# Kernel optimization log

Hardware: AMD Instinct MI355X
Metric: run time of the kernel (lower is better)

## Reference

```python
import jax, jax.numpy as jnp
import numpy as np

SIGMA_S = 1.0
SIGMA_R = 0.1
FR = int(np.ceil(3 * SIGMA_S))          # 3
K_SIZE = 2 * FR + 1                     # 7
B, C, H, W = 8, 3, 512, 512


def matlab_style_gauss2d(shape, sigma):
    m, n = [(ss - 1.0) / 2.0 for ss in shape]
    y, x = np.ogrid[-m:m + 1, -n:n + 1]
    h = np.exp(-(x * x + y * y) / (2.0 * sigma * sigma))
    h[h < np.finfo(h.dtype).eps * h.max()] = 0
    s = h.sum()
    if s != 0:
        h /= s
    return h.astype(np.float32)


GAUSS = matlab_style_gauss2d((K_SIZE, K_SIZE), SIGMA_S)  # [7,7]


def setup_inputs() -> dict:
    key = jax.random.key(0)
    x = jax.random.uniform(key, (B, C, H, W), dtype=jnp.float32)
    return {"input": x}


def reference(input) -> jnp.ndarray:
    # ReflectionPad2d(fr)
    padded = jnp.pad(input, ((0, 0), (0, 0), (FR, FR), (FR, FR)), mode="reflect")
    inv_2sr2 = 1.0 / (2.0 * SIGMA_R * SIGMA_R)
    loss_map = jnp.zeros_like(input)
    for k in range(K_SIZE):
        for l in range(K_SIZE):
            shifted = padded[:, :, k:k + H, l:l + W]            # [B,C,H,W]
            d = input - shifted
            # bilateral range weight * gaussian spatial weight (constant, as in
            # the original which stores weight_map as a raw non-grad tensor)
            w = jax.lax.stop_gradient(
                jnp.exp(-(d * d).sum(1, keepdims=True) * inv_2sr2) * GAUSS[k, l]
            )                                                    # [B,1,H,W]
            loss_map = loss_map + jnp.abs(d) * w
    return loss_map.mean()
```

## Files before the change

### kernel.cpp

```cpp
#include <hip/hip_runtime.h>

#define FR 3
#define KS 7
#define TLX 64
#define TLY 16
#define HX (TLX + 2*FR)
#define HY (TLY + FR)
#define LSTR 72
#define IMG_H 512
#define IMG_W 512
#define NB 8
#define NC 3
#define GXB (IMG_W / TLX)
#define GYB (IMG_H / TLY)
#define NMAIN (GXB * GYB * NB)
#define RIM_PER_IMG 6108
#define NRIM_THREADS (RIM_PER_IMG * NB)
#define NRIM_BLK ((NRIM_THREADS + 255) / 256)
#define NBLK_A (NMAIN + NRIM_BLK)
#define NPART NBLK_A

#define KSC 8.493218f
#define K2F 72.134752f

constexpr double g1d[KS] = {0.011108996538242306, 0.1353352832366127,
                            0.6065306597126334,   1.0,
                            0.6065306597126334,   0.1353352832366127,
                            0.011108996538242306};
constexpr double SUMG = 1.0 + 2.0 * (0.011108996538242306 + 0.1353352832366127
                                     + 0.6065306597126334);
constexpr double INVN = 1.0 / (SUMG * SUMG);
constexpr double KD   = 8.493218;
constexpr double WPAIR = 2.0 * INVN / KD;

__device__ __forceinline__ int refl(int i, int n) {
    i = (i < 0) ? -i : i;
    return (i >= n) ? (2*n - 2 - i) : i;
}

__global__ __launch_bounds__(256) void blt_fused(const float* __restrict__ in,
                                                 float* __restrict__ partial) {
    __shared__ float sm[NC][HY][LSTR];
    __shared__ float wsum[4];
    const int tid = threadIdx.x;
    float a = 0.0f;

    if (blockIdx.x >= NRIM_BLK) {
        const int bid = blockIdx.x - NRIM_BLK;
        const int b   = bid >> 8;
        const int rem = bid & 255;
        const int byi = rem >> 3;
        const int bxi = rem & 7;
        const int by  = byi * TLY;
        const int bx  = bxi * TLX;
        const int tx  = tid & 31;
        const int ty  = tid >> 5;
        const float* base = in + (size_t)b * NC * IMG_H * IMG_W;

        for (int idx = tid; idx < HY * HX; idx += 256) {
            int ly = idx / HX;
            int lx = idx - ly * HX;
            int gy = refl(by + ly - FR, IMG_H);
            int gx = refl(bx + lx - FR, IMG_W);
            #pragma unroll
            for (int c = 0; c < NC; ++c)
                sm[c][ly][lx] = base[(c * IMG_H + gy) * IMG_W + gx] * KSC;
        }
        __syncthreads();

        const int r0 = ty * 2;
        float cc[NC][2][2];

        if ((bxi != 0) & (bxi != GXB - 1) & (byi != 0)) {
            #pragma unroll
            for (int rr = 4; rr >= 0; --rr) {
                float w[NC][8];
                #pragma unroll
                for (int c = 0; c < NC; ++c) {
                    const float2* rp = reinterpret_cast<const float2*>(&sm[c][r0 + rr][2 * tx]);
                    float2 p0 = rp[0], p1 = rp[1], p2 = rp[2], p3 = rp[3];
                    w[c][0] = p0.x; w[c][1] = p0.y; w[c][2] = p1.x; w[c][3] = p1.y;
                    w[c][4] = p2.x; w[c][5] = p2.y; w[c][6] = p3.x; w[c][7] = p3.y;
                }
                #pragma unroll
                for (int i = 0; i < 2; ++i) {
                    const int k = rr - i;
                    if (k < 0 || k > FR) continue;
                    if (k == FR) {
                        #pragma unroll
                        for (int c = 0; c < NC; ++c) {
                            cc[c][i][0] = w[c][3];
                            cc[c][i][1] = w[c][4];
                        }
                    }
                    const int lmax = (k == FR) ? FR : KS;
                    #pragma unroll
                    for (int j = 0; j < 2; ++j) {
                        #pragma unroll
                        for (int l = 0; l < KS; ++l) {
                            if (l >= lmax) continue;
                            float d0 = cc[0][i][j] - w[0][l + j];
                            float d1 = cc[1][i][j] - w[1][l + j];
                            float d2 = cc[2][i][j] - w[2][l + j];
                            float s = d0 * d0;
                            s = fmaf(d1, d1, s);
                            s = fmaf(d2, d2, s);
                            float e = __builtin_amdgcn_exp2f(-s);
                            float sa = fabsf(d0) + fabsf(d1);
                            sa += fabsf(d2);
                            a = fmaf(sa, e * (float)(g1d[k] * g1d[l] * WPAIR), a);
                        }
                    }
                }
            }
        } else {
            const int x0 = bx + 2 * tx;
            float glm0[KS], glm1[KS];
            #pragma unroll
            for (int l = 0; l < KS; ++l) {
                glm0[l] = ((unsigned)(x0 + l - FR)     < (unsigned)IMG_W) ? (float)(g1d[l] * WPAIR) : 0.0f;
                glm1[l] = ((unsigned)(x0 + 1 + l - FR) < (unsigned)IMG_W) ? (float)(g1d[l] * WPAIR) : 0.0f;
            }
            #pragma unroll
            for (int rr = 4; rr >= 0; --rr) {
                float w[NC][8];
                #pragma unroll
                for (int c = 0; c < NC; ++c) {
                    const float2* rp = reinterpret_cast<const float2*>(&sm[c][r0 + rr][2 * tx]);
                    float2 p0 = rp[0], p1 = rp[1], p2 = rp[2], p3 = rp[3];
                    w[c][0] = p0.x; w[c][1] = p0.y; w[c][2] = p1.x; w[c][3] = p1.y;
                    w[c][4] = p2.x; w[c][5] = p2.y; w[c][6] = p3.x; w[c][7] = p3.y;
                }
                #pragma unroll
                for (int i = 0; i < 2; ++i) {
                    const int k = rr - i;
                    if (k < 0 || k > FR) continue;
                    if (k == FR) {
                        #pragma unroll
                        for (int c = 0; c < NC; ++c) {
                            cc[c][i][0] = w[c][3];
                            cc[c][i][1] = w[c][4];
                        }
                    }
                    const int lmax = (k == FR) ? FR : KS;
                    const float rw = (by + r0 + rr >= FR) ? (float)g1d[k] : 0.0f;
                    float t0 = 0.0f, t1 = 0.0f;
                    #pragma unroll
                    for (int l = 0; l < KS; ++l) {
                        if (l >= lmax) continue;
                        {
                            float d0 = cc[0][i][0] - w[0][l];
                            float d1 = cc[1][i][0] - w[1][l];
                            float d2 = cc[2][i][0] - w[2][l];
                            float s = d0 * d0;
                            s = fmaf(d1, d1, s);
                            s = fmaf(d2, d2, s);
                            float e = __builtin_amdgcn_exp2f(-s);
                            float sa = fabsf(d0) + fabsf(d1);
                            sa += fabsf(d2);
                            t0 = fmaf(sa, e * glm0[l], t0);
                        }
                        {
                            float d0 = cc[0][i][1] - w[0][l + 1];
                            float d1 = cc[1][i][1] - w[1][l + 1];
                            float d2 = cc[2][i][1] - w[2][l + 1];
                            float s = d0 * d0;
                            s = fmaf(d1, d1, s);
                            s = fmaf(d2, d2, s);
                            float e = __builtin_amdgcn_exp2f(-s);
                            float sa = fabsf(d0) + fabsf(d1);
                            sa += fabsf(d2);
                            t1 = fmaf(sa, e * glm1[l], t1);
                        }
                    }
                    a = fmaf(t0, rw, a);
                    a = fmaf(t1, rw, a);
                }
            }
        }
    } else {
        const int idx = blockIdx.x * 256 + tid;
        if (idx < NRIM_THREADS) {
            const int b = idx / RIM_PER_IMG;
            int r = idx - b * RIM_PER_IMG;
            int y, x;
            if (r < 3 * IMG_W) { y = r >> 9; x = r & (IMG_W - 1); }
            else if (r < 6 * IMG_W) { r -= 3 * IMG_W; y = (IMG_H - 3) + (r >> 9); x = r & (IMG_W - 1); }
            else if (r < 6 * IMG_W + 3 * (IMG_H - 6)) { r -= 6 * IMG_W; y = 3 + r / 3; x = r - 3 * (r / 3); }
            else { r -= 6 * IMG_W + 3 * (IMG_H - 6); y = 3 + r / 3; x = (IMG_W - 3) + (r - 3 * (r / 3)); }

            const float* base = in + (size_t)b * NC * IMG_H * IMG_W;
            const float cc0 = base[(0 * IMG_H + y) * IMG_W + x];
            const float cc1 = base[(1 * IMG_H + y) * IMG_W + x];
            const float cc2 = base[(2 * IMG_H + y) * IMG_W + x];

            #pragma unroll
            for (int k = 0; k < KS; ++k) {
                #pragma unroll
                for (int l = 0; l < KS; ++l) {
                    if (k == FR && l == FR) continue;
                    int qy = y + k - FR, qx = x + l - FR;
                    bool oob = ((unsigned)qy >= (unsigned)IMG_H) | ((unsigned)qx >= (unsigned)IMG_W);
                    if (oob) {
                        int ry = refl(qy, IMG_H), rx = refl(qx, IMG_W);
                        float v0 = base[(0 * IMG_H + ry) * IMG_W + rx];
                        float v1 = base[(1 * IMG_H + ry) * IMG_W + rx];
                        float v2 = base[(2 * IMG_H + ry) * IMG_W + rx];
                        float d0 = cc0 - v0, d1 = cc1 - v1, d2 = cc2 - v2;
                        float s = d0 * d0;
                        s = fmaf(d1, d1, s);
                        s = fmaf(d2, d2, s);
                        float e = __builtin_amdgcn_exp2f(-(K2F * s));
                        float sa = fabsf(d0) + fabsf(d1) + fabsf(d2);
                        a = fmaf(sa, e * (float)(g1d[k] * g1d[l] * INVN), a);
                    }
                }
            }
        }
        __syncthreads();
    }

    #pragma unroll
    for (int off = 32; off > 0; off >>= 1)
        a += __shfl_down(a, off, 64);
    if ((tid & 63) == 0) wsum[tid >> 6] = a;
    __syncthreads();
    if (tid == 0)
        partial[blockIdx.x] = wsum[0] + wsum[1] + wsum[2] + wsum[3];
}

__global__ __launch_bounds__(256) void finalize_kernel(const float* __restrict__ partial,
                                                       float* __restrict__ out) {
    __shared__ float wsum[4];
    const int tid = threadIdx.x;
    float a = 0.0f;
    for (int i = tid; i < NPART; i += 256) a += partial[i];
    #pragma unroll
    for (int off = 32; off > 0; off >>= 1)
        a += __shfl_down(a, off, 64);
    if ((tid & 63) == 0) wsum[tid >> 6] = a;
    __syncthreads();
    if (tid == 0)
        out[0] = (wsum[0] + wsum[1] + wsum[2] + wsum[3]) / (float)(NB * NC * IMG_H * IMG_W);
}

extern "C" void kernel_launch(void* const* d_in, const int* in_sizes, int n_in,
                              void* d_out, int out_size, void* d_ws, size_t ws_size,
                              hipStream_t stream) {
    const float* in = (const float*)d_in[0];
    float* out = (float*)d_out;
    float* ws  = (float*)d_ws;

    blt_fused<<<NBLK_A, 256, 0, stream>>>(in, ws);
    finalize_kernel<<<1, 256, 0, stream>>>(ws, out);
}
```

Baseline: 90.95 us.

## Group taps by symmetric weight class and fuse final reduction via atomics

In the interior path, per-tap products are accumulated into ten symmetry-class accumulators and multiplied by the class weight once at the end, removing a multiply per tap. The separate finalize kernel is replaced by a global float atomicAdd plus a completion counter, with the last block writing the mean. A hipMemsetAsync is added to clear the accumulator and counter each call. Float atomics make the summation order nondeterministic, and the memset adds its own launch.

```diff
diff --git a/kernel.cpp b/kernel.cpp
--- a/kernel.cpp
+++ b/kernel.cpp
@@ -18,7 +18,6 @@
 #define NRIM_THREADS (RIM_PER_IMG * NB)
 #define NRIM_BLK ((NRIM_THREADS + 255) / 256)
 #define NBLK_A (NMAIN + NRIM_BLK)
-#define NPART NBLK_A
 
 #define KSC 8.493218f
 #define K2F 72.134752f
@@ -33,13 +32,30 @@
 constexpr double KD   = 8.493218;
 constexpr double WPAIR = 2.0 * INVN / KD;
 
+__host__ __device__ constexpr int clsid(int k, int l) {
+    int a = FR - k;
+    int b = (l < FR) ? (FR - l) : (l - FR);
+    int x = a > b ? a : b, y = a > b ? b : a;
+    return x * (x + 1) / 2 + y;
+}
+__host__ __device__ constexpr double gabs(int a) {
+    return (a == 0) ? 1.0 : (a == 1) ? 0.6065306597126334
+         : (a == 2) ? 0.1353352832366127 : 0.011108996538242306;
+}
+__host__ __device__ constexpr double clsw(int id) {
+    int x = (id >= 6) ? 3 : (id >= 3) ? 2 : (id >= 1) ? 1 : 0;
+    int y = id - x * (x + 1) / 2;
+    return gabs(x) * gabs(y) * WPAIR;
+}
+
 __device__ __forceinline__ int refl(int i, int n) {
     i = (i < 0) ? -i : i;
     return (i >= n) ? (2*n - 2 - i) : i;
 }
 
 __global__ __launch_bounds__(256) void blt_fused(const float* __restrict__ in,
-                                                 float* __restrict__ partial) {
+                                                 float* __restrict__ ws,
+                                                 float* __restrict__ out) {
     __shared__ float sm[NC][HY][LSTR];
     __shared__ float wsum[4];
     const int tid = threadIdx.x;
@@ -72,6 +88,10 @@
         float cc[NC][2][2];
 
         if ((bxi != 0) & (bxi != GXB - 1) & (byi != 0)) {
+            float t[10];
+            #pragma unroll
+            for (int c = 0; c < 10; ++c) t[c] = 0.0f;
+
             #pragma unroll
             for (int rr = 4; rr >= 0; --rr) {
                 float w[NC][8];
@@ -108,11 +128,14 @@
                             float e = __builtin_amdgcn_exp2f(-s);
                             float sa = fabsf(d0) + fabsf(d1);
                             sa += fabsf(d2);
-                            a = fmaf(sa, e * (float)(g1d[k] * g1d[l] * WPAIR), a);
-                        }
-                    }
-                }
-            }
+                            t[clsid(k, l)] = fmaf(sa, e, t[clsid(k, l)]);
+                        }
+                    }
+                }
+            }
+            #pragma unroll
+            for (int c = 0; c < 10; ++c)
+                a = fmaf(t[c], (float)clsw(c), a);
         } else {
             const int x0 = bx + 2 * tx;
             float glm0[KS], glm1[KS];
@@ -225,23 +248,16 @@
         a += __shfl_down(a, off, 64);
     if ((tid & 63) == 0) wsum[tid >> 6] = a;
     __syncthreads();
-    if (tid == 0)
-        partial[blockIdx.x] = wsum[0] + wsum[1] + wsum[2] + wsum[3];
-}
-
-__global__ __launch_bounds__(256) void finalize_kernel(const float* __restrict__ partial,
-                                                       float* __restrict__ out) {
-    __shared__ float wsum[4];
-    const int tid = threadIdx.x;
-    float a = 0.0f;
-    for (int i = tid; i < NPART; i += 256) a += partial[i];
-    #pragma unroll
-    for (int off = 32; off > 0; off >>= 1)
-        a += __shfl_down(a, off, 64);
-    if ((tid & 63) == 0) wsum[tid >> 6] = a;
-    __syncthreads();
-    if (tid == 0)
-        out[0] = (wsum[0] + wsum[1] + wsum[2] + wsum[3]) / (float)(NB * NC * IMG_H * IMG_W);
+    if (tid == 0) {
+        float blocksum = wsum[0] + wsum[1] + wsum[2] + wsum[3];
+        atomicAdd(&ws[0], blocksum);
+        __threadfence();
+        unsigned old = atomicAdd((unsigned*)&ws[1], 1u);
+        if (old == (unsigned)(NBLK_A - 1)) {
+            float total = atomicAdd(&ws[0], 0.0f);
+            out[0] = total * (1.0f / (float)(NB * NC * IMG_H * IMG_W));
+        }
+    }
 }
 
 extern "C" void kernel_launch(void* const* d_in, const int* in_sizes, int n_in,
@@ -251,6 +267,6 @@
     float* out = (float*)d_out;
     float* ws  = (float*)d_ws;
 
-    blt_fused<<<NBLK_A, 256, 0, stream>>>(in, ws);
-    finalize_kernel<<<1, 256, 0, stream>>>(ws, out);
-}
+    hipMemsetAsync(ws, 0, 2 * sizeof(float), stream);
+    blt_fused<<<NBLK_A, 256, 0, stream>>>(in, ws, out);
+}
```

Result: slower. 133.0 us (+46.2%).
